# Optimization experiments

Measured on AMD Instinct MI355X. Metric: run time of the kernel, lower is better.

The kernel has to match this reference:

```python
import jax, jax.numpy as jnp
import numpy as np

N_PTS = 524288
N_LEVELS = 16
F_PER = 2
T = 1 << 19            # log2_hashmap_size = 19
BASE_RES = 16
BOUND = 1.0
PLS = float(np.exp2(np.log2(2048.0 * BOUND / N_LEVELS) / (N_LEVELS - 1)))
RES = [int(np.floor(BASE_RES * PLS ** l)) for l in range(N_LEVELS)]
OFFS = np.array([[(i >> 2) & 1, (i >> 1) & 1, i & 1] for i in range(8)], dtype=np.int32)  # [8,3] cube corners


def hashgrid_encode(x, tables):
    # x: [N,3] in [0,1]; tables: [L, T, F]
    offs = jnp.asarray(OFFS)
    offs_b = offs.astype(bool)
    feats = []
    for l in range(N_LEVELS):
        res = RES[l]
        pos = x * (res - 1)
        p0 = jnp.floor(pos)
        frac = pos - p0                                     # [N,3]
        corners = jnp.clip(p0.astype(jnp.int32)[:, None, :] + offs[None], 0, res - 1)  # [N,8,3]
        w = jnp.prod(jnp.where(offs_b[None], frac[:, None, :], 1.0 - frac[:, None, :]), axis=-1)  # [N,8]
        if res ** 3 <= T:
            idx = corners[..., 0] + res * corners[..., 1] + res * res * corners[..., 2]
        else:
            c = corners.astype(jnp.uint32)
            idx = (c[..., 0] ^ (c[..., 1] * jnp.uint32(2654435761)) ^ (c[..., 2] * jnp.uint32(805459861))) & jnp.uint32(T - 1)
            idx = idx.astype(jnp.int32)
        feats.append(jnp.einsum('nkf,nk->nf', tables[l][idx], w))  # trilinear interp
    return jnp.concatenate(feats, axis=-1)  # [N, 32]


def sh_encode(d):
    # degree-4 spherical harmonics basis, torch-ngp coefficients -> [N,16]
    x, y, z = d[..., 0], d[..., 1], d[..., 2]
    xy, xz, yz = x * y, x * z, y * z
    x2, y2, z2 = x * x, y * y, z * z
    return jnp.stack([
        jnp.full_like(x, 0.28209479177387814),
        -0.48860251190291987 * y,
        0.48860251190291987 * z,
        -0.48860251190291987 * x,
        1.0925484305920792 * xy,
        -1.0925484305920792 * yz,
        0.94617469575755997 * z2 - 0.31539156525252005,
        -1.0925484305920792 * xz,
        0.54627421529603959 * (x2 - y2),
        0.59004358992664352 * y * (-3.0 * x2 + y2),
        2.8906114426405538 * xy * z,
        0.45704579946446572 * y * (1.0 - 5.0 * z2),
        0.3731763325901154 * z * (5.0 * z2 - 3.0),
        0.45704579946446572 * x * (1.0 - 5.0 * z2),
        1.4453057213202769 * z * (x2 - y2),
        0.59004358992664352 * x * (x2 - 3.0 * y2),
    ], axis=-1)


def l2_normalize(v):
    return v / jnp.maximum(jnp.linalg.norm(v, axis=-1, keepdims=True), 1e-8)


def density(xyz, tables, ws0, ws1):
    xn = jnp.clip((xyz + BOUND) / (2.0 * BOUND), 0.0, 1.0)
    h = jax.nn.relu(hashgrid_encode(xn, tables) @ ws0)  # [N,64]
    h = h @ ws1                                          # [N,16]
    return h[..., 0], h[..., 1:]                         # sigma [N], geo_feat [N,15]


def setup_inputs() -> dict:
    key = jax.random.key(0)
    ks = jax.random.split(key, 11)
    x = jax.random.uniform(ks[0], (N_PTS, 6), minval=-1.0, maxval=1.0, dtype=jnp.float32)
    tables = jax.random.uniform(ks[1], (N_LEVELS, T, F_PER), minval=-1e-4, maxval=1e-4, dtype=jnp.float32)

    def lin(k, din, dout):
        s = 1.0 / float(np.sqrt(din))
        return jax.random.uniform(k, (din, dout), minval=-s, maxval=s, dtype=jnp.float32)

    return dict(
        x=x, tables=tables,
        ws0=lin(ks[2], 32, 64), ws1=lin(ks[3], 64, 16),
        wc0=lin(ks[4], 31, 64), wc1=lin(ks[5], 64, 64), wc2=lin(ks[6], 64, 3),
        wn0=lin(ks[7], 15, 64), wn1=lin(ks[8], 64, 3),
        wm0=lin(ks[9], 15, 32), bm0=jnp.zeros((32,), jnp.float32),
        wm1=lin(ks[10], 32, 1), bm1=jnp.zeros((1,), jnp.float32),
    )


def reference(x, tables, ws0, ws1, wc0, wc1, wc2, wn0, wn1, wm0, bm0, wm1, bm1):
    xyz, d = x[:, :3], x[:, 3:]

    # sigma + analytic normal = l2_normalize(-grad_x sigma)  (compute_normal=True path)
    def f(p):
        s, g = density(p, tables, ws0, ws1)
        return s.sum(), (s, g)

    (_, (sigma, geo_feat)), grad_density = jax.value_and_grad(f, has_aux=True)(xyz)
    normal = l2_normalize(-grad_density)

    # predicted normal head (bias-free 15->64->3)
    pred_normal = l2_normalize(jax.nn.relu(geo_feat @ wn0) @ wn1)

    # color head: SH(dir) ++ geo_feat -> 31->64->64->3, sigmoid
    h = jnp.concatenate([sh_encode(d), geo_feat], axis=-1)
    rgb = jax.nn.sigmoid(jax.nn.relu(jax.nn.relu(h @ wc0) @ wc1) @ wc2)

    # mirror-mask head: 15->32 LeakyReLU ->1 sigmoid (with biases)
    m = jax.nn.leaky_relu(geo_feat @ wm0 + bm0, negative_slope=0.01)
    is_mirror = jax.nn.sigmoid(m @ wm1 + bm1)

    return sigma, geo_feat, normal, pred_normal, rgb, is_mirror
```

## Files before the change

### kernel.cpp

```cpp
#include <hip/hip_runtime.h>
#include <math.h>

#define N_POINTS 524288
#define NLV      16
#define TSZ      524288
#define TMASK    (TSZ - 1)
#define ASTART   5
#define NA       (NLV - ASTART)

static_assert(NA == 11, "NA mismatch");

struct Params { int res[NLV]; };


struct Gather {
    float2 t0, t1, t2, t3, t4, t5, t6, t7;
    float fx, fy, fz;
};
struct Enc2 { float e0, e1; };
struct EncA { float e0, e1, a0x, a0y, a0z, a1x, a1y, a1z; };
struct L3v  { float lx, ly, lz; };

__device__ __forceinline__ Gather lv_issue_rt(const float2* __restrict__ lt, const int res,
                                              const bool hashed,
                                              const float xn0, const float xn1, const float xn2)
{
#pragma clang fp contract(off)
    Gather g;
    const float rf = (float)(res - 1);
    const float px = xn0 * rf, py = xn1 * rf, pz = xn2 * rf;
    const float bx = floorf(px), by = floorf(py), bz = floorf(pz);
    g.fx = px - bx; g.fy = py - by; g.fz = pz - bz;
    const int r1 = res - 1;
    const int ix = (int)bx, iy = (int)by, iz = (int)bz;
    const int cx0 = min(max(ix, 0), r1),     cx1 = min(max(ix + 1, 0), r1);
    const int cy0 = min(max(iy, 0), r1),     cy1 = min(max(iy + 1, 0), r1);
    const int cz0 = min(max(iz, 0), r1),     cz1 = min(max(iz + 1, 0), r1);
    unsigned i000, i001, i010, i011, i100, i101, i110, i111;
    if (hashed) {
        const unsigned hx0 = (unsigned)cx0, hx1 = (unsigned)cx1;
        const unsigned hy0 = (unsigned)cy0 * 2654435761u, hy1 = (unsigned)cy1 * 2654435761u;
        const unsigned hz0 = (unsigned)cz0 * 805459861u,  hz1 = (unsigned)cz1 * 805459861u;
        const unsigned e00 = hy0 ^ hz0, e01 = hy0 ^ hz1, e10 = hy1 ^ hz0, e11 = hy1 ^ hz1;
        i000 = (hx0 ^ e00) & TMASK; i001 = (hx0 ^ e01) & TMASK;
        i010 = (hx0 ^ e10) & TMASK; i011 = (hx0 ^ e11) & TMASK;
        i100 = (hx1 ^ e00) & TMASK; i101 = (hx1 ^ e01) & TMASK;
        i110 = (hx1 ^ e10) & TMASK; i111 = (hx1 ^ e11) & TMASK;
    } else {
        const int b00 = res * (cy0 + res * cz0), b01 = res * (cy0 + res * cz1);
        const int b10 = res * (cy1 + res * cz0), b11 = res * (cy1 + res * cz1);
        i000 = (unsigned)(cx0 + b00); i001 = (unsigned)(cx0 + b01);
        i010 = (unsigned)(cx0 + b10); i011 = (unsigned)(cx0 + b11);
        i100 = (unsigned)(cx1 + b00); i101 = (unsigned)(cx1 + b01);
        i110 = (unsigned)(cx1 + b10); i111 = (unsigned)(cx1 + b11);
    }
    g.t0 = lt[i000]; g.t1 = lt[i001]; g.t2 = lt[i010]; g.t3 = lt[i011];
    g.t4 = lt[i100]; g.t5 = lt[i101]; g.t6 = lt[i110]; g.t7 = lt[i111];
    return g;
}

template<bool HASHED>
__device__ __forceinline__ Gather lv_issue(const float2* __restrict__ lt, const int res,
                                           const float xn0, const float xn1, const float xn2)
{
    return lv_issue_rt(lt, res, HASHED, xn0, xn1, xn2);
}

__device__ __forceinline__ Enc2 lv_enc(const Gather g)
{
#pragma clang fp contract(off)
    const float gx0 = 1.0f - g.fx, gx1 = g.fx;
    const float gy0 = 1.0f - g.fy, gy1 = g.fy;
    const float gz0 = 1.0f - g.fz, gz1 = g.fz;
    const float pxy00 = gx0 * gy0, pxy01 = gx0 * gy1, pxy10 = gx1 * gy0, pxy11 = gx1 * gy1;
    const float w000 = pxy00 * gz0, w001 = pxy00 * gz1, w010 = pxy01 * gz0, w011 = pxy01 * gz1;
    const float w100 = pxy10 * gz0, w101 = pxy10 * gz1, w110 = pxy11 * gz0, w111 = pxy11 * gz1;
    float e0 = 0.0f, e1 = 0.0f;
    e0 = e0 + w000 * g.t0.x; e1 = e1 + w000 * g.t0.y;
    e0 = e0 + w001 * g.t1.x; e1 = e1 + w001 * g.t1.y;
    e0 = e0 + w010 * g.t2.x; e1 = e1 + w010 * g.t2.y;
    e0 = e0 + w011 * g.t3.x; e1 = e1 + w011 * g.t3.y;
    e0 = e0 + w100 * g.t4.x; e1 = e1 + w100 * g.t4.y;
    e0 = e0 + w101 * g.t5.x; e1 = e1 + w101 * g.t5.y;
    e0 = e0 + w110 * g.t6.x; e1 = e1 + w110 * g.t6.y;
    e0 = e0 + w111 * g.t7.x; e1 = e1 + w111 * g.t7.y;
    Enc2 r; r.e0 = e0; r.e1 = e1; return r;
}

__device__ __forceinline__ EncA lv_enc_a(const Gather g)
{
#pragma clang fp contract(off)
    const float gx0 = 1.0f - g.fx, gx1 = g.fx;
    const float gy0 = 1.0f - g.fy, gy1 = g.fy;
    const float gz0 = 1.0f - g.fz, gz1 = g.fz;
    const float pxy00 = gx0 * gy0, pxy01 = gx0 * gy1, pxy10 = gx1 * gy0, pxy11 = gx1 * gy1;
    const float w000 = pxy00 * gz0, w001 = pxy00 * gz1, w010 = pxy01 * gz0, w011 = pxy01 * gz1;
    const float w100 = pxy10 * gz0, w101 = pxy10 * gz1, w110 = pxy11 * gz0, w111 = pxy11 * gz1;
    float e0 = 0.0f, e1 = 0.0f;
    e0 = e0 + w000 * g.t0.x; e1 = e1 + w000 * g.t0.y;
    e0 = e0 + w001 * g.t1.x; e1 = e1 + w001 * g.t1.y;
    e0 = e0 + w010 * g.t2.x; e1 = e1 + w010 * g.t2.y;
    e0 = e0 + w011 * g.t3.x; e1 = e1 + w011 * g.t3.y;
    e0 = e0 + w100 * g.t4.x; e1 = e1 + w100 * g.t4.y;
    e0 = e0 + w101 * g.t5.x; e1 = e1 + w101 * g.t5.y;
    e0 = e0 + w110 * g.t6.x; e1 = e1 + w110 * g.t6.y;
    e0 = e0 + w111 * g.t7.x; e1 = e1 + w111 * g.t7.y;
    const float pyz00 = gy0 * gz0, pyz01 = gy0 * gz1, pyz10 = gy1 * gz0, pyz11 = gy1 * gz1;
    const float pxz00 = gx0 * gz0, pxz01 = gx0 * gz1, pxz10 = gx1 * gz0, pxz11 = gx1 * gz1;
    float a0x = 0.f, a0y = 0.f, a0z = 0.f, a1x = 0.f, a1y = 0.f, a1z = 0.f;
    a0x = fmaf(-pyz00, g.t0.x, a0x); a1x = fmaf(-pyz00, g.t0.y, a1x);
    a0y = fmaf(-pxz00, g.t0.x, a0y); a1y = fmaf(-pxz00, g.t0.y, a1y);
    a0z = fmaf(-pxy00, g.t0.x, a0z); a1z = fmaf(-pxy00, g.t0.y, a1z);
    a0x = fmaf(-pyz01, g.t1.x, a0x); a1x = fmaf(-pyz01, g.t1.y, a1x);
    a0y = fmaf(-pxz01, g.t1.x, a0y); a1y = fmaf(-pxz01, g.t1.y, a1y);
    a0z = fmaf( pxy00, g.t1.x, a0z); a1z = fmaf( pxy00, g.t1.y, a1z);
    a0x = fmaf(-pyz10, g.t2.x, a0x); a1x = fmaf(-pyz10, g.t2.y, a1x);
    a0y = fmaf( pxz00, g.t2.x, a0y); a1y = fmaf( pxz00, g.t2.y, a1y);
    a0z = fmaf(-pxy01, g.t2.x, a0z); a1z = fmaf(-pxy01, g.t2.y, a1z);
    a0x = fmaf(-pyz11, g.t3.x, a0x); a1x = fmaf(-pyz11, g.t3.y, a1x);
    a0y = fmaf( pxz01, g.t3.x, a0y); a1y = fmaf( pxz01, g.t3.y, a1y);
    a0z = fmaf( pxy01, g.t3.x, a0z); a1z = fmaf( pxy01, g.t3.y, a1z);
    a0x = fmaf( pyz00, g.t4.x, a0x); a1x = fmaf( pyz00, g.t4.y, a1x);
    a0y = fmaf(-pxz10, g.t4.x, a0y); a1y = fmaf(-pxz10, g.t4.y, a1y);
    a0z = fmaf(-pxy10, g.t4.x, a0z); a1z = fmaf(-pxy10, g.t4.y, a1z);
    a0x = fmaf( pyz01, g.t5.x, a0x); a1x = fmaf( pyz01, g.t5.y, a1x);
    a0y = fmaf(-pxz11, g.t5.x, a0y); a1y = fmaf(-pxz11, g.t5.y, a1y);
    a0z = fmaf( pxy10, g.t5.x, a0z); a1z = fmaf( pxy10, g.t5.y, a1z);
    a0x = fmaf( pyz10, g.t6.x, a0x); a1x = fmaf( pyz10, g.t6.y, a1x);
    a0y = fmaf( pxz10, g.t6.x, a0y); a1y = fmaf( pxz10, g.t6.y, a1y);
    a0z = fmaf(-pxy11, g.t6.x, a0z); a1z = fmaf(-pxy11, g.t6.y, a1z);
    a0x = fmaf( pyz11, g.t7.x, a0x); a1x = fmaf( pyz11, g.t7.y, a1x);
    a0y = fmaf( pxz11, g.t7.x, a0y); a1y = fmaf( pxz11, g.t7.y, a1y);
    a0z = fmaf( pxy11, g.t7.x, a0z); a1z = fmaf( pxy11, g.t7.y, a1z);
    EncA r;
    r.e0 = e0; r.e1 = e1;
    r.a0x = a0x; r.a0y = a0y; r.a0z = a0z;
    r.a1x = a1x; r.a1y = a1y; r.a1z = a1z;
    return r;
}

__device__ __forceinline__ L3v bwd_part(const Gather g, const float g0, const float g1)
{
    const float gx0 = 1.0f - g.fx, gx1 = g.fx;
    const float gy0 = 1.0f - g.fy, gy1 = g.fy;
    const float gz0 = 1.0f - g.fz, gz1 = g.fz;
    const float pyz00 = gy0 * gz0, pyz01 = gy0 * gz1, pyz10 = gy1 * gz0, pyz11 = gy1 * gz1;
    const float pxz00 = gx0 * gz0, pxz01 = gx0 * gz1, pxz10 = gx1 * gz0, pxz11 = gx1 * gz1;
    const float pxy00 = gx0 * gy0, pxy01 = gx0 * gy1, pxy10 = gx1 * gy0, pxy11 = gx1 * gy1;
    const float s000 = fmaf(g0, g.t0.x, g1 * g.t0.y);
    const float s001 = fmaf(g0, g.t1.x, g1 * g.t1.y);
    const float s010 = fmaf(g0, g.t2.x, g1 * g.t2.y);
    const float s011 = fmaf(g0, g.t3.x, g1 * g.t3.y);
    const float s100 = fmaf(g0, g.t4.x, g1 * g.t4.y);
    const float s101 = fmaf(g0, g.t5.x, g1 * g.t5.y);
    const float s110 = fmaf(g0, g.t6.x, g1 * g.t6.y);
    const float s111 = fmaf(g0, g.t7.x, g1 * g.t7.y);
    float lx = 0.f, ly = 0.f, lz = 0.f;
    lx = fmaf(-pyz00, s000, lx); ly = fmaf(-pxz00, s000, ly); lz = fmaf(-pxy00, s000, lz);
    lx = fmaf(-pyz01, s001, lx); ly = fmaf(-pxz01, s001, ly); lz = fmaf( pxy00, s001, lz);
    lx = fmaf(-pyz10, s010, lx); ly = fmaf( pxz00, s010, ly); lz = fmaf(-pxy01, s010, lz);
    lx = fmaf(-pyz11, s011, lx); ly = fmaf( pxz01, s011, ly); lz = fmaf( pxy01, s011, lz);
    lx = fmaf( pyz00, s100, lx); ly = fmaf(-pxz10, s100, ly); lz = fmaf(-pxy10, s100, lz);
    lx = fmaf( pyz01, s101, lx); ly = fmaf(-pxz11, s101, ly); lz = fmaf( pxy10, s101, lz);
    lx = fmaf( pyz10, s110, lx); ly = fmaf( pxz10, s110, ly); lz = fmaf(-pxy11, s110, lz);
    lx = fmaf( pyz11, s111, lx); ly = fmaf( pxz11, s111, ly); lz = fmaf( pxy11, s111, lz);
    L3v r; r.lx = lx; r.ly = ly; r.lz = lz; return r;
}

__device__ __forceinline__ void clampedxn(const float* __restrict__ x, const int n,
                                          float& xn0, float& xn1, float& xn2)
{
    const float x0 = x[(size_t)n * 6 + 0];
    const float x1 = x[(size_t)n * 6 + 1];
    const float x2 = x[(size_t)n * 6 + 2];
    xn0 = fminf(fmaxf((x0 + 1.0f) * 0.5f, 0.0f), 1.0f);
    xn1 = fminf(fmaxf((x1 + 1.0f) * 0.5f, 0.0f), 1.0f);
    xn2 = fminf(fmaxf((x2 + 1.0f) * 0.5f, 0.0f), 1.0f);
}

__global__ __launch_bounds__(256) __attribute__((amdgpu_waves_per_eu(8, 8)))
void k_gather_phased(const float* __restrict__ x, const float* __restrict__ tables,
                     float* __restrict__ ws, Params P)
{
    const int lvl = blockIdx.x >> 11;
    const int n = ((blockIdx.x & 2047) << 8) + threadIdx.x;
    if (n >= N_POINTS) return;
    const size_t N = (size_t)N_POINTS;
    float xn0, xn1, xn2;
    clampedxn(x, n, xn0, xn1, xn2);
    const float2* __restrict__ tb = (const float2*)tables;
    float* __restrict__ we = ws;
    float* __restrict__ wa = ws + 32 * N;

    const int res = P.res[lvl];
    const bool hashed = (long long)res * res * res > (long long)TSZ;
    const Gather g = lv_issue_rt(tb + (size_t)lvl * TSZ, res, hashed, xn0, xn1, xn2);

    if (lvl >= ASTART) {
        const EncA r = lv_enc_a(g);
        we[(size_t)(2 * lvl) * N + n] = r.e0;
        we[(size_t)(2 * lvl + 1) * N + n] = r.e1;
        const int i_ = lvl - ASTART;
        wa[(size_t)(0 * NA + i_) * N + n] = r.a0x;
        wa[(size_t)(1 * NA + i_) * N + n] = r.a0y;
        wa[(size_t)(2 * NA + i_) * N + n] = r.a0z;
        wa[(size_t)(3 * NA + i_) * N + n] = r.a1x;
        wa[(size_t)(4 * NA + i_) * N + n] = r.a1y;
        wa[(size_t)(5 * NA + i_) * N + n] = r.a1z;
    } else {
        const Enc2 r = lv_enc(g);
        we[(size_t)(2 * lvl) * N + n] = r.e0;
        we[(size_t)(2 * lvl + 1) * N + n] = r.e1;
    }
}

__global__ __launch_bounds__(256) __attribute__((amdgpu_waves_per_eu(4, 4)))
void k_density(const float* __restrict__ x, const float* __restrict__ tables,
               const float* __restrict__ w_s0, const float* __restrict__ w_s1,
               const float* __restrict__ ws, float* __restrict__ wgeo,
               float* __restrict__ out, Params P)
{
    const int n = blockIdx.x * 256 + threadIdx.x;
    if (n >= N_POINTS) return;
    const size_t N = (size_t)N_POINTS;
    float xn0, xn1, xn2;
    clampedxn(x, n, xn0, xn1, xn2);
    const float2* __restrict__ tb = (const float2*)tables;
    const float* __restrict__ we = ws;
    const float* __restrict__ wa = ws + 32 * N;

    float enc[32];
    #pragma unroll
    for (int j = 0; j < 32; ++j) enc[j] = we[(size_t)j * N + n];

    float hd[16];
    #pragma unroll
    for (int m = 0; m < 16; ++m) hd[m] = 0.0f;
    unsigned long long mask = 0ull;
    {
        #pragma clang fp contract(off)
        for (int k = 0; k < 64; ++k) {
            float a = 0.0f;
            #pragma unroll
            for (int j = 0; j < 32; ++j) {
                const float p = enc[j] * w_s0[j * 64 + k];
                a = a + p;
            }
            const float hr = fmaxf(a, 0.0f);
            #pragma unroll
            for (int m = 0; m < 16; ++m) hd[m] = fmaf(hr, w_s1[k * 16 + m], hd[m]);
            if (a > 0.0f) mask |= (1ull << k);
        }
    }
    const float sigma = hd[0];

    out[n] = sigma;
    #pragma unroll
    for (int j = 0; j < 15; ++j) {
        out[N + (size_t)n * 15 + j] = hd[1 + j];
        wgeo[(size_t)j * N + n] = hd[1 + j];
    }

    float genc[32];
    #pragma unroll
    for (int j = 0; j < 32; ++j) genc[j] = 0.0f;
    for (int k = 0; k < 64; ++k) {
        const float ghk = ((mask >> k) & 1ull) ? w_s1[k * 16] : 0.0f;
        #pragma unroll
        for (int j = 0; j < 32; ++j) genc[j] = fmaf(w_s0[j * 64 + k], ghk, genc[j]);
    }

    float gx = 0.0f, gy = 0.0f, gz = 0.0f;
    {
        const Gather gA = lv_issue<false>(tb + 0 * (size_t)TSZ, P.res[0], xn0, xn1, xn2);
        const Gather gB = lv_issue<false>(tb + 1 * (size_t)TSZ, P.res[1], xn0, xn1, xn2);
        {
            const L3v d = bwd_part(gA, genc[0], genc[1]);
            const float rf = (float)(P.res[0] - 1);
            gx = fmaf(d.lx, rf, gx); gy = fmaf(d.ly, rf, gy); gz = fmaf(d.lz, rf, gz);
        }
        {
            const L3v d = bwd_part(gB, genc[2], genc[3]);
            const float rf = (float)(P.res[1] - 1);
            gx = fmaf(d.lx, rf, gx); gy = fmaf(d.ly, rf, gy); gz = fmaf(d.lz, rf, gz);
        }
    }
    {
        const Gather gA = lv_issue<false>(tb + 2 * (size_t)TSZ, P.res[2], xn0, xn1, xn2);
        const Gather gB = lv_issue<false>(tb + 3 * (size_t)TSZ, P.res[3], xn0, xn1, xn2);
        {
            const L3v d = bwd_part(gA, genc[4], genc[5]);
            const float rf = (float)(P.res[2] - 1);
            gx = fmaf(d.lx, rf, gx); gy = fmaf(d.ly, rf, gy); gz = fmaf(d.lz, rf, gz);
        }
        {
            const L3v d = bwd_part(gB, genc[6], genc[7]);
            const float rf = (float)(P.res[3] - 1);
            gx = fmaf(d.lx, rf, gx); gy = fmaf(d.ly, rf, gy); gz = fmaf(d.lz, rf, gz);
        }
    }
    {
        const Gather gA = lv_issue<false>(tb + 4 * (size_t)TSZ, P.res[4], xn0, xn1, xn2);
        const L3v d = bwd_part(gA, genc[8], genc[9]);
        const float rf = (float)(P.res[4] - 1);
        gx = fmaf(d.lx, rf, gx); gy = fmaf(d.ly, rf, gy); gz = fmaf(d.lz, rf, gz);
    }

    #pragma unroll
    for (int l = ASTART; l < NLV; ++l) {
        const int i = l - ASTART;
        const float rf = (float)(P.res[l] - 1);
        const float g0 = genc[2 * l], g1 = genc[2 * l + 1];
        const float a0x = wa[(size_t)(0*NA + i)*N + n];
        const float a0y = wa[(size_t)(1*NA + i)*N + n];
        const float a0z = wa[(size_t)(2*NA + i)*N + n];
        const float a1x = wa[(size_t)(3*NA + i)*N + n];
        const float a1y = wa[(size_t)(4*NA + i)*N + n];
        const float a1z = wa[(size_t)(5*NA + i)*N + n];
        gx = fmaf(rf, fmaf(g0, a0x, g1 * a1x), gx);
        gy = fmaf(rf, fmaf(g0, a0y, g1 * a1y), gy);
        gz = fmaf(rf, fmaf(g0, a0z, g1 * a1z), gz);
    }
    gx *= 0.5f; gy *= 0.5f; gz *= 0.5f;

    const float gnorm = sqrtf(gx * gx + gy * gy + gz * gz);
    const float ginv = 1.0f / fmaxf(gnorm, 1e-8f);

    out[16 * N + (size_t)n * 3 + 0] = -gx * ginv;
    out[16 * N + (size_t)n * 3 + 1] = -gy * ginv;
    out[16 * N + (size_t)n * 3 + 2] = -gz * ginv;
}

__global__ __launch_bounds__(256) __attribute__((amdgpu_waves_per_eu(4, 4)))
void k_color(const float* __restrict__ x,
             const float* __restrict__ wc0, const float* __restrict__ wc1,
             const float* __restrict__ wc2,
             const float* __restrict__ wn0, const float* __restrict__ wn1,
             const float* __restrict__ wm0, const float* __restrict__ bm0,
             const float* __restrict__ wm1, const float* __restrict__ bm1,
             const float* __restrict__ wgeo, float* __restrict__ out)
{
    const int n = blockIdx.x * 256 + threadIdx.x;
    if (n >= N_POINTS) return;
    const size_t N = (size_t)N_POINTS;

    float geo[15];
    #pragma unroll
    for (int j = 0; j < 15; ++j) geo[j] = wgeo[(size_t)j * N + n];

    float pn0 = 0.0f, pn1 = 0.0f, pn2 = 0.0f;
    for (int k = 0; k < 64; ++k) {
        float a = 0.0f;
        #pragma unroll
        for (int j = 0; j < 15; ++j) a = fmaf(geo[j], wn0[j * 64 + k], a);
        a = fmaxf(a, 0.0f);
        pn0 = fmaf(a, wn1[k * 3 + 0], pn0);
        pn1 = fmaf(a, wn1[k * 3 + 1], pn1);
        pn2 = fmaf(a, wn1[k * 3 + 2], pn2);
    }
    const float pnorm = sqrtf(pn0 * pn0 + pn1 * pn1 + pn2 * pn2);
    const float pinv = 1.0f / fmaxf(pnorm, 1e-8f);
    out[19 * N + (size_t)n * 3 + 0] = pn0 * pinv;
    out[19 * N + (size_t)n * 3 + 1] = pn1 * pinv;
    out[19 * N + (size_t)n * 3 + 2] = pn2 * pinv;

    float macc = 0.0f;
    for (int k = 0; k < 32; ++k) {
        float a = bm0[k];
        #pragma unroll
        for (int j = 0; j < 15; ++j) a = fmaf(geo[j], wm0[j * 32 + k], a);
        a = (a >= 0.0f) ? a : 0.01f * a;
        macc = fmaf(a, wm1[k], macc);
    }
    macc += bm1[0];
    out[25 * N + n] = 1.0f / (1.0f + expf(-macc));

    const float dx = x[(size_t)n * 6 + 3];
    const float dy = x[(size_t)n * 6 + 4];
    const float dz = x[(size_t)n * 6 + 5];
    float sh[16];
    const float xy = dx * dy, xz = dx * dz, yz = dy * dz;
    const float x2s = dx * dx, y2s = dy * dy, z2s = dz * dz;
    sh[0]  = 0.28209479177387814f;
    sh[1]  = -0.48860251190291987f * dy;
    sh[2]  =  0.48860251190291987f * dz;
    sh[3]  = -0.48860251190291987f * dx;
    sh[4]  =  1.0925484305920792f * xy;
    sh[5]  = -1.0925484305920792f * yz;
    sh[6]  =  0.94617469575756f * z2s - 0.31539156525252005f;
    sh[7]  = -1.0925484305920792f * xz;
    sh[8]  =  0.5462742152960396f * (x2s - y2s);
    sh[9]  =  0.5900435899266435f * dy * (-3.0f * x2s + y2s);
    sh[10] =  2.890611442640554f * xy * dz;
    sh[11] =  0.4570457994644657f * dy * (1.0f - 5.0f * z2s);
    sh[12] =  0.3731763325901154f * dz * (5.0f * z2s - 3.0f);
    sh[13] =  0.4570457994644657f * dx * (1.0f - 5.0f * z2s);
    sh[14] =  1.445305721320277f * dz * (x2s - y2s);
    sh[15] =  0.5900435899266435f * dx * (x2s - 3.0f * y2s);

    float cacc[64];
    #pragma unroll
    for (int k = 0; k < 64; ++k) cacc[k] = 0.0f;
    for (int kc = 0; kc < 64; ++kc) {
        float a = 0.0f;
        #pragma unroll
        for (int j = 0; j < 16; ++j) a = fmaf(sh[j], wc0[j * 64 + kc], a);
        #pragma unroll
        for (int j = 0; j < 15; ++j) a = fmaf(geo[j], wc0[(16 + j) * 64 + kc], a);
        const float c1v = fmaxf(a, 0.0f);
        const float* __restrict__ wrow = wc1 + kc * 64;
        #pragma unroll
        for (int k2 = 0; k2 < 64; ++k2) cacc[k2] = fmaf(c1v, wrow[k2], cacc[k2]);
    }
    float r0 = 0.0f, r1 = 0.0f, r2 = 0.0f;
    #pragma unroll
    for (int k = 0; k < 64; ++k) {
        const float a = fmaxf(cacc[k], 0.0f);
        r0 = fmaf(a, wc2[k * 3 + 0], r0);
        r1 = fmaf(a, wc2[k * 3 + 1], r1);
        r2 = fmaf(a, wc2[k * 3 + 2], r2);
    }
    out[22 * N + (size_t)n * 3 + 0] = 1.0f / (1.0f + expf(-r0));
    out[22 * N + (size_t)n * 3 + 1] = 1.0f / (1.0f + expf(-r1));
    out[22 * N + (size_t)n * 3 + 2] = 1.0f / (1.0f + expf(-r2));
}

__global__ __launch_bounds__(256) __attribute__((amdgpu_waves_per_eu(3, 4)))
void nerf_mono(const float* __restrict__ x, const float* __restrict__ tables,
               const float* __restrict__ w_s0, const float* __restrict__ w_s1,
               const float* __restrict__ wc0, const float* __restrict__ wc1,
               const float* __restrict__ wc2, const float* __restrict__ wn0,
               const float* __restrict__ wn1, const float* __restrict__ wm0,
               const float* __restrict__ bm0, const float* __restrict__ wm1,
               const float* __restrict__ bm1, float* __restrict__ out, Params P)
{
    const int n = blockIdx.x * 256 + threadIdx.x;
    if (n >= N_POINTS) return;
    float xn0, xn1, xn2;
    clampedxn(x, n, xn0, xn1, xn2);
    const float2* __restrict__ tb = (const float2*)tables;

    float enc[32];
    float A0x[NA], A0y[NA], A0z[NA], A1x[NA], A1y[NA], A1z[NA];

#define MPAIR_NN(LA, LB) {                                                             \
        const Gather gA = lv_issue<false>(tb + (size_t)(LA)*TSZ, P.res[LA], xn0, xn1, xn2); \
        const Gather gB = lv_issue<false>(tb + (size_t)(LB)*TSZ, P.res[LB], xn0, xn1, xn2); \
        const Enc2 rA = lv_enc(gA); enc[2*(LA)] = rA.e0; enc[2*(LA)+1] = rA.e1;        \
        const Enc2 rB = lv_enc(gB); enc[2*(LB)] = rB.e0; enc[2*(LB)+1] = rB.e1; }
#define MPAIR_NA(LA, LB) {                                                             \
        const Gather gA = lv_issue<false>(tb + (size_t)(LA)*TSZ, P.res[LA], xn0, xn1, xn2); \
        const Gather gB = lv_issue<false>(tb + (size_t)(LB)*TSZ, P.res[LB], xn0, xn1, xn2); \
        const Enc2 rA = lv_enc(gA); enc[2*(LA)] = rA.e0; enc[2*(LA)+1] = rA.e1;        \
        const EncA rB = lv_enc_a(gB); enc[2*(LB)] = rB.e0; enc[2*(LB)+1] = rB.e1;      \
        A0x[(LB)-ASTART] = rB.a0x; A0y[(LB)-ASTART] = rB.a0y; A0z[(LB)-ASTART] = rB.a0z; \
        A1x[(LB)-ASTART] = rB.a1x; A1y[(LB)-ASTART] = rB.a1y; A1z[(LB)-ASTART] = rB.a1z; }
#define MPAIR_AA(LA, LB) {                                                             \
        const Gather gA = lv_issue<true>(tb + (size_t)(LA)*TSZ, P.res[LA], xn0, xn1, xn2);  \
        const Gather gB = lv_issue<true>(tb + (size_t)(LB)*TSZ, P.res[LB], xn0, xn1, xn2);  \
        const EncA rA = lv_enc_a(gA); enc[2*(LA)] = rA.e0; enc[2*(LA)+1] = rA.e1;      \
        A0x[(LA)-ASTART] = rA.a0x; A0y[(LA)-ASTART] = rA.a0y; A0z[(LA)-ASTART] = rA.a0z; \
        A1x[(LA)-ASTART] = rA.a1x; A1y[(LA)-ASTART] = rA.a1y; A1z[(LA)-ASTART] = rA.a1z; \
        const EncA rB = lv_enc_a(gB); enc[2*(LB)] = rB.e0; enc[2*(LB)+1] = rB.e1;      \
        A0x[(LB)-ASTART] = rB.a0x; A0y[(LB)-ASTART] = rB.a0y; A0z[(LB)-ASTART] = rB.a0z; \
        A1x[(LB)-ASTART] = rB.a1x; A1y[(LB)-ASTART] = rB.a1y; A1z[(LB)-ASTART] = rB.a1z; }

    MPAIR_NN(0, 1)
    MPAIR_NN(2, 3)
    MPAIR_NA(4, 5)
    MPAIR_AA(6, 7)
    MPAIR_AA(8, 9)
    MPAIR_AA(10, 11)
    MPAIR_AA(12, 13)
    MPAIR_AA(14, 15)
#undef MPAIR_NN
#undef MPAIR_NA
#undef MPAIR_AA

    float hd[16];
    #pragma unroll
    for (int m = 0; m < 16; ++m) hd[m] = 0.0f;
    unsigned long long mask = 0ull;
    {
        #pragma clang fp contract(off)
        for (int k = 0; k < 64; ++k) {
            float a = 0.0f;
            #pragma unroll
            for (int j = 0; j < 32; ++j) {
                const float p = enc[j] * w_s0[j * 64 + k];
                a = a + p;
            }
            const float hr = fmaxf(a, 0.0f);
            #pragma unroll
            for (int m = 0; m < 16; ++m) hd[m] = fmaf(hr, w_s1[k * 16 + m], hd[m]);
            if (a > 0.0f) mask |= (1ull << k);
        }
    }
    const float sigma = hd[0];

    float gx = 0.0f, gy = 0.0f, gz = 0.0f;
    {
        const Gather g0v = lv_issue<false>(tb + 0 * (size_t)TSZ, P.res[0], xn0, xn1, xn2);
        const Gather g1v = lv_issue<false>(tb + 1 * (size_t)TSZ, P.res[1], xn0, xn1, xn2);

        float genc[32];
        #pragma unroll
        for (int j = 0; j < 32; ++j) genc[j] = 0.0f;
        for (int k = 0; k < 64; ++k) {
            const float ghk = ((mask >> k) & 1ull) ? w_s1[k * 16] : 0.0f;
            #pragma unroll
            for (int j = 0; j < 32; ++j) genc[j] = fmaf(w_s0[j * 64 + k], ghk, genc[j]);
        }

        {
            const L3v d = bwd_part(g0v, genc[0], genc[1]);
            const float rf = (float)(P.res[0] - 1);
            gx = fmaf(d.lx, rf, gx); gy = fmaf(d.ly, rf, gy); gz = fmaf(d.lz, rf, gz);
        }
        {
            const L3v d = bwd_part(g1v, genc[2], genc[3]);
            const float rf = (float)(P.res[1] - 1);
            gx = fmaf(d.lx, rf, gx); gy = fmaf(d.ly, rf, gy); gz = fmaf(d.lz, rf, gz);
        }
        {
            const Gather g2v = lv_issue<false>(tb + 2 * (size_t)TSZ, P.res[2], xn0, xn1, xn2);
            const Gather g3v = lv_issue<false>(tb + 3 * (size_t)TSZ, P.res[3], xn0, xn1, xn2);
            {
                const L3v d = bwd_part(g2v, genc[4], genc[5]);
                const float rf = (float)(P.res[2] - 1);
                gx = fmaf(d.lx, rf, gx); gy = fmaf(d.ly, rf, gy); gz = fmaf(d.lz, rf, gz);
            }
            {
                const L3v d = bwd_part(g3v, genc[6], genc[7]);
                const float rf = (float)(P.res[3] - 1);
                gx = fmaf(d.lx, rf, gx); gy = fmaf(d.ly, rf, gy); gz = fmaf(d.lz, rf, gz);
            }
        }
        {
            const Gather g4v = lv_issue<false>(tb + 4 * (size_t)TSZ, P.res[4], xn0, xn1, xn2);
            const L3v d = bwd_part(g4v, genc[8], genc[9]);
            const float rf = (float)(P.res[4] - 1);
            gx = fmaf(d.lx, rf, gx); gy = fmaf(d.ly, rf, gy); gz = fmaf(d.lz, rf, gz);
        }

        #pragma unroll
        for (int l = ASTART; l < NLV; ++l) {
            const int i = l - ASTART;
            const float rf = (float)(P.res[l] - 1);
            const float g0 = genc[2 * l], g1 = genc[2 * l + 1];
            gx = fmaf(rf, fmaf(g0, A0x[i], g1 * A1x[i]), gx);
            gy = fmaf(rf, fmaf(g0, A0y[i], g1 * A1y[i]), gy);
            gz = fmaf(rf, fmaf(g0, A0z[i], g1 * A1z[i]), gz);
        }
    }
    gx *= 0.5f; gy *= 0.5f; gz *= 0.5f;

    const float gnorm = sqrtf(gx * gx + gy * gy + gz * gz);
    const float ginv = 1.0f / fmaxf(gnorm, 1e-8f);

    float geo[15];
    #pragma unroll
    for (int j = 0; j < 15; ++j) geo[j] = hd[1 + j];

    float pn0 = 0.0f, pn1 = 0.0f, pn2 = 0.0f;
    for (int k = 0; k < 64; ++k) {
        float a = 0.0f;
        #pragma unroll
        for (int j = 0; j < 15; ++j) a = fmaf(geo[j], wn0[j * 64 + k], a);
        a = fmaxf(a, 0.0f);
        pn0 = fmaf(a, wn1[k * 3 + 0], pn0);
        pn1 = fmaf(a, wn1[k * 3 + 1], pn1);
        pn2 = fmaf(a, wn1[k * 3 + 2], pn2);
    }
    const float pnorm = sqrtf(pn0 * pn0 + pn1 * pn1 + pn2 * pn2);
    const float pinv = 1.0f / fmaxf(pnorm, 1e-8f);

    const float dx = x[(size_t)n * 6 + 3];
    const float dy = x[(size_t)n * 6 + 4];
    const float dz = x[(size_t)n * 6 + 5];
    float sh[16];
    const float xy = dx * dy, xz = dx * dz, yz = dy * dz;
    const float x2s = dx * dx, y2s = dy * dy, z2s = dz * dz;
    sh[0]  = 0.28209479177387814f;
    sh[1]  = -0.48860251190291987f * dy;
    sh[2]  =  0.48860251190291987f * dz;
    sh[3]  = -0.48860251190291987f * dx;
    sh[4]  =  1.0925484305920792f * xy;
    sh[5]  = -1.0925484305920792f * yz;
    sh[6]  =  0.94617469575756f * z2s - 0.31539156525252005f;
    sh[7]  = -1.0925484305920792f * xz;
    sh[8]  =  0.5462742152960396f * (x2s - y2s);
    sh[9]  =  0.5900435899266435f * dy * (-3.0f * x2s + y2s);
    sh[10] =  2.890611442640554f * xy * dz;
    sh[11] =  0.4570457994644657f * dy * (1.0f - 5.0f * z2s);
    sh[12] =  0.3731763325901154f * dz * (5.0f * z2s - 3.0f);
    sh[13] =  0.4570457994644657f * dx * (1.0f - 5.0f * z2s);
    sh[14] =  1.445305721320277f * dz * (x2s - y2s);
    sh[15] =  0.5900435899266435f * dx * (x2s - 3.0f * y2s);

    float cacc[64];
    #pragma unroll
    for (int k = 0; k < 64; ++k) cacc[k] = 0.0f;
    for (int kc = 0; kc < 64; ++kc) {
        float a = 0.0f;
        #pragma unroll
        for (int j = 0; j < 16; ++j) a = fmaf(sh[j], wc0[j * 64 + kc], a);
        #pragma unroll
        for (int j = 0; j < 15; ++j) a = fmaf(geo[j], wc0[(16 + j) * 64 + kc], a);
        const float c1v = fmaxf(a, 0.0f);
        const float* __restrict__ wrow = wc1 + kc * 64;
        #pragma unroll
        for (int k2 = 0; k2 < 64; ++k2) cacc[k2] = fmaf(c1v, wrow[k2], cacc[k2]);
    }
    float r0 = 0.0f, r1 = 0.0f, r2 = 0.0f;
    #pragma unroll
    for (int k = 0; k < 64; ++k) {
        const float a = fmaxf(cacc[k], 0.0f);
        r0 = fmaf(a, wc2[k * 3 + 0], r0);
        r1 = fmaf(a, wc2[k * 3 + 1], r1);
        r2 = fmaf(a, wc2[k * 3 + 2], r2);
    }
    const float rgb0 = 1.0f / (1.0f + expf(-r0));
    const float rgb1 = 1.0f / (1.0f + expf(-r1));
    const float rgb2 = 1.0f / (1.0f + expf(-r2));

    float macc = 0.0f;
    for (int k = 0; k < 32; ++k) {
        float a = bm0[k];
        #pragma unroll
        for (int j = 0; j < 15; ++j) a = fmaf(geo[j], wm0[j * 32 + k], a);
        a = (a >= 0.0f) ? a : 0.01f * a;
        macc = fmaf(a, wm1[k], macc);
    }
    macc += bm1[0];
    const float mir = 1.0f / (1.0f + expf(-macc));

    const size_t N = (size_t)N_POINTS;
    out[n] = sigma;
    #pragma unroll
    for (int j = 0; j < 15; ++j)
        out[N + (size_t)n * 15 + j] = geo[j];
    out[16 * N + (size_t)n * 3 + 0] = -gx * ginv;
    out[16 * N + (size_t)n * 3 + 1] = -gy * ginv;
    out[16 * N + (size_t)n * 3 + 2] = -gz * ginv;
    out[19 * N + (size_t)n * 3 + 0] = pn0 * pinv;
    out[19 * N + (size_t)n * 3 + 1] = pn1 * pinv;
    out[19 * N + (size_t)n * 3 + 2] = pn2 * pinv;
    out[22 * N + (size_t)n * 3 + 0] = rgb0;
    out[22 * N + (size_t)n * 3 + 1] = rgb1;
    out[22 * N + (size_t)n * 3 + 2] = rgb2;
    out[25 * N + n] = mir;
}

extern "C" void kernel_launch(void* const* d_in, const int* in_sizes, int n_in,
                              void* d_out, int out_size, void* d_ws, size_t ws_size,
                              hipStream_t stream)
{
    Params P;
    const double PLS = exp2(log2(2048.0 * 1.0 / 16.0) / 15.0);
    for (int l = 0; l < NLV; ++l)
        P.res[l] = (int)floor(16.0 * pow(PLS, (double)l));

    const float* x      = (const float*)d_in[0];
    const float* tables = (const float*)d_in[1];
    const float* w_s0   = (const float*)d_in[2];
    const float* w_s1   = (const float*)d_in[3];
    const float* wc0    = (const float*)d_in[4];
    const float* wc1    = (const float*)d_in[5];
    const float* wc2    = (const float*)d_in[6];
    const float* wn0    = (const float*)d_in[7];
    const float* wn1    = (const float*)d_in[8];
    const float* wm0    = (const float*)d_in[9];
    const float* bm0    = (const float*)d_in[10];
    const float* wm1    = (const float*)d_in[11];
    const float* bm1    = (const float*)d_in[12];
    float* out = (float*)d_out;

    const size_t N = (size_t)N_POINTS;
    const size_t need = (size_t)(32 + 66 + 15) * N * sizeof(float);

    if (d_ws != nullptr && ws_size >= need) {
        float* ws   = (float*)d_ws;
        float* wgeo = ws + (size_t)98 * N;
        k_gather_phased<<<NLV * (N_POINTS / 256), 256, 0, stream>>>(x, tables, ws, P);
        k_density<<<N_POINTS / 256, 256, 0, stream>>>(x, tables, w_s0, w_s1,
                                                      ws, wgeo, out, P);
        k_color  <<<N_POINTS / 256, 256, 0, stream>>>(x, wc0, wc1, wc2,
                                                      wn0, wn1, wm0, bm0, wm1, bm1,
                                                      wgeo, out);
    } else {
        nerf_mono<<<N_POINTS / 256, 256, 0, stream>>>(x, tables, w_s0, w_s1,
                                                      wc0, wc1, wc2, wn0, wn1,
                                                      wm0, bm0, wm1, bm1, out, P);
    }
}
```

Baseline: 770.4 us.

## Merge dense levels into one gather phase and split density kernel into MLP and backward

The gather kernel now launches 11 phases instead of 16. Phase 0 handles the six dense levels together in pairs, and the other phases each handle one hashed level with compile-time hashing flags. The density kernel is split in two. k_dmlp runs the forward MLP and stores the ReLU mask into the workspace slots of the already consumed level-0 encodings. k_bwd reads that mask and does the analytic-gradient backward pass with table re-gathers. The goal is to cut per-level launch and branch overhead and give each kernel better occupancy. In exchange it adds a kernel launch and relies on overwriting workspace that k_bwd must not read as encodings.

```diff
diff --git a/kernel.cpp b/kernel.cpp
--- a/kernel.cpp
+++ b/kernel.cpp
@@ -7,6 +7,7 @@
 #define TMASK    (TSZ - 1)
 #define ASTART   5
 #define NA       (NLV - ASTART)
+#define NPH      11
 
 static_assert(NA == 11, "NA mismatch");
 
@@ -182,7 +183,7 @@
 void k_gather_phased(const float* __restrict__ x, const float* __restrict__ tables,
                      float* __restrict__ ws, Params P)
 {
-    const int lvl = blockIdx.x >> 11;
+    const int ph = blockIdx.x >> 11;
     const int n = ((blockIdx.x & 2047) << 8) + threadIdx.x;
     if (n >= N_POINTS) return;
     const size_t N = (size_t)N_POINTS;
@@ -192,42 +193,55 @@
     float* __restrict__ we = ws;
     float* __restrict__ wa = ws + 32 * N;
 
-    const int res = P.res[lvl];
-    const bool hashed = (long long)res * res * res > (long long)TSZ;
-    const Gather g = lv_issue_rt(tb + (size_t)lvl * TSZ, res, hashed, xn0, xn1, xn2);
-
-    if (lvl >= ASTART) {
+#define ST_E(L, R) { we[(size_t)(2*(L))*N + n] = R.e0; we[(size_t)(2*(L)+1)*N + n] = R.e1; }
+#define ST_A(L, R) { const int i_ = (L) - ASTART;                         \
+        wa[(size_t)(0*NA + i_)*N + n] = R.a0x;                            \
+        wa[(size_t)(1*NA + i_)*N + n] = R.a0y;                            \
+        wa[(size_t)(2*NA + i_)*N + n] = R.a0z;                            \
+        wa[(size_t)(3*NA + i_)*N + n] = R.a1x;                            \
+        wa[(size_t)(4*NA + i_)*N + n] = R.a1y;                            \
+        wa[(size_t)(5*NA + i_)*N + n] = R.a1z; }
+
+    if (ph == 0) {
+        {
+            const Gather gA = lv_issue_rt(tb + 0 * (size_t)TSZ, P.res[0], false, xn0, xn1, xn2);
+            const Gather gB = lv_issue_rt(tb + 1 * (size_t)TSZ, P.res[1], false, xn0, xn1, xn2);
+            const Enc2 rA = lv_enc(gA); ST_E(0, rA)
+            const Enc2 rB = lv_enc(gB); ST_E(1, rB)
+        }
+        {
+            const Gather gA = lv_issue_rt(tb + 2 * (size_t)TSZ, P.res[2], false, xn0, xn1, xn2);
+            const Gather gB = lv_issue_rt(tb + 3 * (size_t)TSZ, P.res[3], false, xn0, xn1, xn2);
+            const Enc2 rA = lv_enc(gA); ST_E(2, rA)
+            const Enc2 rB = lv_enc(gB); ST_E(3, rB)
+        }
+        {
+            const Gather gA = lv_issue_rt(tb + 4 * (size_t)TSZ, P.res[4], false, xn0, xn1, xn2);
+            const Gather gB = lv_issue_rt(tb + 5 * (size_t)TSZ, P.res[5], false, xn0, xn1, xn2);
+            const Enc2 rA = lv_enc(gA); ST_E(4, rA)
+            const EncA rB = lv_enc_a(gB); ST_E(5, rB) ST_A(5, rB)
+        }
+    } else {
+        const int lvl = 5 + ph;
+        const Gather g = lv_issue_rt(tb + (size_t)lvl * TSZ, P.res[lvl], true, xn0, xn1, xn2);
         const EncA r = lv_enc_a(g);
-        we[(size_t)(2 * lvl) * N + n] = r.e0;
-        we[(size_t)(2 * lvl + 1) * N + n] = r.e1;
-        const int i_ = lvl - ASTART;
-        wa[(size_t)(0 * NA + i_) * N + n] = r.a0x;
-        wa[(size_t)(1 * NA + i_) * N + n] = r.a0y;
-        wa[(size_t)(2 * NA + i_) * N + n] = r.a0z;
-        wa[(size_t)(3 * NA + i_) * N + n] = r.a1x;
-        wa[(size_t)(4 * NA + i_) * N + n] = r.a1y;
-        wa[(size_t)(5 * NA + i_) * N + n] = r.a1z;
-    } else {
-        const Enc2 r = lv_enc(g);
-        we[(size_t)(2 * lvl) * N + n] = r.e0;
-        we[(size_t)(2 * lvl + 1) * N + n] = r.e1;
-    }
-}
-
-__global__ __launch_bounds__(256) __attribute__((amdgpu_waves_per_eu(4, 4)))
-void k_density(const float* __restrict__ x, const float* __restrict__ tables,
-               const float* __restrict__ w_s0, const float* __restrict__ w_s1,
-               const float* __restrict__ ws, float* __restrict__ wgeo,
-               float* __restrict__ out, Params P)
+        ST_E(lvl, r)
+        ST_A(lvl, r)
+    }
+#undef ST_E
+#undef ST_A
+}
+
+__global__ __launch_bounds__(256) __attribute__((amdgpu_waves_per_eu(6, 8)))
+void k_dmlp(const float* __restrict__ x,
+            const float* __restrict__ w_s0, const float* __restrict__ w_s1,
+            float* __restrict__ ws, float* __restrict__ wgeo,
+            float* __restrict__ out)
 {
     const int n = blockIdx.x * 256 + threadIdx.x;
     if (n >= N_POINTS) return;
     const size_t N = (size_t)N_POINTS;
-    float xn0, xn1, xn2;
-    clampedxn(x, n, xn0, xn1, xn2);
-    const float2* __restrict__ tb = (const float2*)tables;
-    const float* __restrict__ we = ws;
-    const float* __restrict__ wa = ws + 32 * N;
+    float* __restrict__ we = ws;
 
     float enc[32];
     #pragma unroll
@@ -252,14 +266,34 @@
             if (a > 0.0f) mask |= (1ull << k);
         }
     }
-    const float sigma = hd[0];
-
-    out[n] = sigma;
+
+    out[n] = hd[0];
     #pragma unroll
     for (int j = 0; j < 15; ++j) {
         out[N + (size_t)n * 15 + j] = hd[1 + j];
         wgeo[(size_t)j * N + n] = hd[1 + j];
     }
+    we[(size_t)0 * N + n] = __uint_as_float((unsigned)(mask & 0xffffffffull));
+    we[(size_t)1 * N + n] = __uint_as_float((unsigned)(mask >> 32));
+}
+
+__global__ __launch_bounds__(256) __attribute__((amdgpu_waves_per_eu(4, 8)))
+void k_bwd(const float* __restrict__ x, const float* __restrict__ tables,
+           const float* __restrict__ w_s0, const float* __restrict__ w_s1,
+           const float* __restrict__ ws, float* __restrict__ out, Params P)
+{
+    const int n = blockIdx.x * 256 + threadIdx.x;
+    if (n >= N_POINTS) return;
+    const size_t N = (size_t)N_POINTS;
+    float xn0, xn1, xn2;
+    clampedxn(x, n, xn0, xn1, xn2);
+    const float2* __restrict__ tb = (const float2*)tables;
+    const float* __restrict__ we = ws;
+    const float* __restrict__ wa = ws + 32 * N;
+
+    const unsigned mlo = __float_as_uint(we[(size_t)0 * N + n]);
+    const unsigned mhi = __float_as_uint(we[(size_t)1 * N + n]);
+    const unsigned long long mask = ((unsigned long long)mhi << 32) | mlo;
 
     float genc[32];
     #pragma unroll
@@ -682,12 +716,12 @@
     if (d_ws != nullptr && ws_size >= need) {
         float* ws   = (float*)d_ws;
         float* wgeo = ws + (size_t)98 * N;
-        k_gather_phased<<<NLV * (N_POINTS / 256), 256, 0, stream>>>(x, tables, ws, P);
-        k_density<<<N_POINTS / 256, 256, 0, stream>>>(x, tables, w_s0, w_s1,
-                                                      ws, wgeo, out, P);
-        k_color  <<<N_POINTS / 256, 256, 0, stream>>>(x, wc0, wc1, wc2,
-                                                      wn0, wn1, wm0, bm0, wm1, bm1,
-                                                      wgeo, out);
+        k_gather_phased<<<NPH * (N_POINTS / 256), 256, 0, stream>>>(x, tables, ws, P);
+        k_dmlp <<<N_POINTS / 256, 256, 0, stream>>>(x, w_s0, w_s1, ws, wgeo, out);
+        k_bwd  <<<N_POINTS / 256, 256, 0, stream>>>(x, tables, w_s0, w_s1, ws, out, P);
+        k_color<<<N_POINTS / 256, 256, 0, stream>>>(x, wc0, wc1, wc2,
+                                                    wn0, wn1, wm0, bm0, wm1, bm1,
+                                                    wgeo, out);
     } else {
         nerf_mono<<<N_POINTS / 256, 256, 0, stream>>>(x, tables, w_s0, w_s1,
                                                       wc0, wc1, wc2, wn0, wn1,
```

After: 794.1 us. 3.1% more time.
